# Kernel tuning notes

Hardware: AMD Instinct MI355X
Metric: run time of the kernel (lower is better)

The kernel has to match this reference:

```python
import jax, jax.numpy as jnp
import numpy as np

N, F_IN, H, OUT, E = 1_000_000, 8, 32, 9, 4_000_000


def setup_inputs() -> dict:
    key = jax.random.key(0)
    ks = jax.random.split(key, 32)
    s = 0.05
    inp = {
        "x": jax.random.normal(ks[0], (N, F_IN), jnp.float32),
        "edge_index": jax.random.randint(ks[1], (2, E), 0, N, jnp.int64),
        "edge_weight": jax.random.uniform(ks[2], (E,), jnp.float32),
        "h": jax.random.normal(ks[3], (N, H), jnp.float32),
        "c": jax.random.normal(ks[4], (N, H), jnp.float32),
    }
    i = 5
    # per-gate ChebConv(K=1) weights on x and h, peephole vectors, gate biases
    for g in ["i", "f", "c", "o"]:
        inp[f"Wx{g}"] = jax.random.normal(ks[i], (F_IN, H), jnp.float32) * s; i += 1
        inp[f"bx{g}"] = jnp.zeros((H,), jnp.float32)
        inp[f"Wh{g}"] = jax.random.normal(ks[i], (H, H), jnp.float32) * s; i += 1
        inp[f"bh{g}"] = jnp.zeros((H,), jnp.float32)
        inp[f"b{g}"] = jnp.zeros((H,), jnp.float32)
        if g != "c":  # cell candidate gate has no peephole
            inp[f"wc{g}"] = jax.random.normal(ks[i], (H,), jnp.float32) * s; i += 1
    inp["Wl"] = jax.random.normal(ks[i], (H, OUT), jnp.float32) * s
    inp["bl"] = jnp.zeros((OUT,), jnp.float32)
    return inp


def reference(x, edge_index, edge_weight, h, c,
              Wxi, bxi, Whi, bhi, bi, wci,
              Wxf, bxf, Whf, bhf, bf, wcf,
              Wxc, bxc, Whc, bhc, bc,
              Wxo, bxo, Who, bho, bo, wco,
              Wl, bl):
    # GConvLSTM with ChebConv K=1: graph conv degenerates to x @ W + b
    # (edge_index / edge_weight do not enter the math for K=1).
    i_g = jax.nn.sigmoid(x @ Wxi + bxi + h @ Whi + bhi + wci * c + bi)
    f_g = jax.nn.sigmoid(x @ Wxf + bxf + h @ Whf + bhf + wcf * c + bf)
    t_g = jnp.tanh(x @ Wxc + bxc + h @ Whc + bhc + bc)
    c0 = f_g * c + i_g * t_g
    o_g = jax.nn.sigmoid(x @ Wxo + bxo + h @ Who + bho + wco * c0 + bo)
    h0 = o_g * jnp.tanh(c0)
    y = jax.nn.relu(h0) @ Wl + bl  # [N, 9]
    return (y, h0, c0)
```

## Files before the change

### kernel.cpp

```cpp
#include <hip/hip_runtime.h>
#include <math.h>


#define HD 32
#define FD 8
#define BLK 256

struct Params {
    const float* __restrict__ x;
    const float* __restrict__ h;
    const float* __restrict__ c;
    const float* __restrict__ Wx[4];
    const float* __restrict__ bx[4];
    const float* __restrict__ Wh[4];
    const float* __restrict__ bh[4];
    const float* __restrict__ b[4];
    const float* __restrict__ wci;
    const float* __restrict__ wcf;
    const float* __restrict__ wco;
    const float* __restrict__ Wl;
    const float* __restrict__ bl;
    float* __restrict__ y;
    float* __restrict__ h0;
    float* __restrict__ c0;
    int N;
};

__device__ __forceinline__ float rcp_f(float x) { return __builtin_amdgcn_rcpf(x); }
__device__ __forceinline__ float fsigmoid(float x) { return rcp_f(1.0f + __expf(-x)); }
__device__ __forceinline__ float ftanh(float x) {
    float e = __expf(2.0f * fabsf(x));
    float r = 1.0f - 2.0f * rcp_f(1.0f + e);
    return copysignf(r, x);
}

__global__ __launch_bounds__(BLK) void gconvlstm_kernel(Params p) {
    __shared__ __align__(16) float WXT[4][HD][FD];
    __shared__ __align__(16) float WHT[4][HD][HD];
    __shared__ __align__(16) float WLT[HD][12];
    __shared__ __align__(16) float SCV[HD][8];

    const int tid = threadIdx.x;

    for (int t = tid; t < 4 * HD * FD; t += BLK) {
        int g = t >> 8, r = t & 255, j = r >> 3, k = r & 7;
        WXT[g][j][k] = p.Wx[g][k * HD + j];
    }
    for (int t = tid; t < 4 * HD * HD; t += BLK) {
        int g = t >> 10, r = t & 1023, j = r >> 5, k = r & 31;
        WHT[g][j][k] = p.Wh[g][k * HD + j];
    }
    for (int t = tid; t < HD * 12; t += BLK) {
        int j = t / 12, m = t - j * 12;
        WLT[j][m] = (m < 9) ? p.Wl[j * 9 + m] : 0.0f;
    }
    for (int t = tid; t < HD * 8; t += BLK) {
        int j = t >> 3, s = t & 7;
        float v = 0.0f;
        if (s < 4)      v = p.bx[s][j] + p.bh[s][j] + p.b[s][j];
        else if (s == 4) v = p.wci[j];
        else if (s == 5) v = p.wcf[j];
        else if (s == 6) v = p.wco[j];
        SCV[j][s] = v;
    }
    __syncthreads();

    const int n = blockIdx.x * BLK + tid;
    if (n >= p.N) return;

    float xv[FD], hv[HD], cv[HD], h0a[HD];

    const float4* xp = reinterpret_cast<const float4*>(p.x + (size_t)n * FD);
    reinterpret_cast<float4*>(xv)[0] = xp[0];
    reinterpret_cast<float4*>(xv)[1] = xp[1];
    const float4* hp = reinterpret_cast<const float4*>(p.h + (size_t)n * HD);
#pragma unroll
    for (int q = 0; q < 8; ++q) reinterpret_cast<float4*>(hv)[q] = hp[q];
    const float4* cp = reinterpret_cast<const float4*>(p.c + (size_t)n * HD);
#pragma unroll
    for (int q = 0; q < 8; ++q) reinterpret_cast<float4*>(cv)[q] = cp[q];

    float yacc[9];
#pragma unroll
    for (int m = 0; m < 9; ++m) yacc[m] = p.bl[m];

#pragma unroll
    for (int j = 0; j < HD; ++j) {
        float ai = 0.f, af = 0.f, at = 0.f, ao = 0.f;
#pragma unroll
        for (int k = 0; k < FD; ++k) {
            ai += xv[k] * WXT[0][j][k];
            af += xv[k] * WXT[1][j][k];
            at += xv[k] * WXT[2][j][k];
            ao += xv[k] * WXT[3][j][k];
        }
#pragma unroll
        for (int k = 0; k < HD; ++k) {
            ai += hv[k] * WHT[0][j][k];
            af += hv[k] * WHT[1][j][k];
            at += hv[k] * WHT[2][j][k];
            ao += hv[k] * WHT[3][j][k];
        }
        const float cj = cv[j];
        const float pi = ai + SCV[j][0] + SCV[j][4] * cj;
        const float pf = af + SCV[j][1] + SCV[j][5] * cj;
        const float pt = at + SCV[j][2];
        const float ig = fsigmoid(pi);
        const float fg = fsigmoid(pf);
        const float tg = ftanh(pt);
        const float c0 = fg * cj + ig * tg;
        const float po = ao + SCV[j][3] + SCV[j][6] * c0;
        const float og = fsigmoid(po);
        const float h0 = og * ftanh(c0);
        cv[j] = c0;
        h0a[j] = h0;
        const float rh = fmaxf(h0, 0.0f);
#pragma unroll
        for (int m = 0; m < 9; ++m) yacc[m] += rh * WLT[j][m];
    }

    float* yo = p.y + (size_t)n * 9;
#pragma unroll
    for (int m = 0; m < 9; ++m) yo[m] = yacc[m];
    float4* ho = reinterpret_cast<float4*>(p.h0 + (size_t)n * HD);
#pragma unroll
    for (int q = 0; q < 8; ++q) ho[q] = reinterpret_cast<const float4*>(h0a)[q];
    float4* co = reinterpret_cast<float4*>(p.c0 + (size_t)n * HD);
#pragma unroll
    for (int q = 0; q < 8; ++q) co[q] = reinterpret_cast<const float4*>(cv)[q];
}

extern "C" void kernel_launch(void* const* d_in, const int* in_sizes, int n_in,
                              void* d_out, int out_size, void* d_ws, size_t ws_size,
                              hipStream_t stream) {
    (void)n_in; (void)d_ws; (void)ws_size;
    const int N = in_sizes[0] / FD;

    Params p;
    p.x = (const float*)d_in[0];
    p.h = (const float*)d_in[3];
    p.c = (const float*)d_in[4];

    const int wx_i[4] = {5, 11, 17, 22};
    const int bx_i[4] = {6, 12, 18, 23};
    const int wh_i[4] = {7, 13, 19, 24};
    const int bh_i[4] = {8, 14, 20, 25};
    const int b_i[4]  = {9, 15, 21, 26};
    for (int g = 0; g < 4; ++g) {
        p.Wx[g] = (const float*)d_in[wx_i[g]];
        p.bx[g] = (const float*)d_in[bx_i[g]];
        p.Wh[g] = (const float*)d_in[wh_i[g]];
        p.bh[g] = (const float*)d_in[bh_i[g]];
        p.b[g]  = (const float*)d_in[b_i[g]];
    }
    p.wci = (const float*)d_in[10];
    p.wcf = (const float*)d_in[16];
    p.wco = (const float*)d_in[27];
    p.Wl  = (const float*)d_in[28];
    p.bl  = (const float*)d_in[29];

    float* out = (float*)d_out;
    p.y  = out;
    p.h0 = out + (size_t)9 * N;
    p.c0 = out + (size_t)41 * N;
    p.N  = N;

    const int blocks = (N + BLK - 1) / BLK;
    gconvlstm_kernel<<<blocks, BLK, 0, stream>>>(p);
}
```

Measured before the change: 772.4 us.

## Pre-transpose weights into workspace and read them via uniform scalar loads

A one-block prep kernel transposes and packs all gate weights, fused biases, peepholes and the output layer into a workspace buffer. The main kernel no longer stages weights in shared memory or syncs, and reads them straight from global memory with wave-uniform addresses, which the compiler can turn into scalar loads. The cell state is now streamed one float4 at a time and outputs are written per chunk, which lowers register pressure. tanh also uses a cheaper formula. The cost is an extra kernel launch, plus a heavy dependence on the scalar cache for about 5.7K weight reads per thread.

New measurement: 968.6 us. +25.4%, slower.

```diff
diff --git a/kernel.cpp b/kernel.cpp
--- a/kernel.cpp
+++ b/kernel.cpp
@@ -6,165 +6,166 @@
 #define FD 8
 #define BLK 256
 
-struct Params {
-    const float* __restrict__ x;
-    const float* __restrict__ h;
-    const float* __restrict__ c;
-    const float* __restrict__ Wx[4];
-    const float* __restrict__ bx[4];
-    const float* __restrict__ Wh[4];
-    const float* __restrict__ bh[4];
-    const float* __restrict__ b[4];
-    const float* __restrict__ wci;
-    const float* __restrict__ wcf;
-    const float* __restrict__ wco;
-    const float* __restrict__ Wl;
-    const float* __restrict__ bl;
-    float* __restrict__ y;
-    float* __restrict__ h0;
-    float* __restrict__ c0;
-    int N;
+#define CW_WXT 0
+#define CW_WHT 1024
+#define CW_WL  5120
+#define CW_B   5504
+#define CW_PCI 5632
+#define CW_PCF 5664
+#define CW_PCO 5696
+#define CW_BL  5728
+#define CW_TOT 5740
+
+struct PrepArgs {
+    const float* Wxi; const float* Wxf; const float* Wxc; const float* Wxo;
+    const float* Whi; const float* Whf; const float* Whc; const float* Who;
+    const float* bxi; const float* bxf; const float* bxc; const float* bxo;
+    const float* bhi; const float* bhf; const float* bhc; const float* bho;
+    const float* bi;  const float* bf;  const float* bc;  const float* bo;
+    const float* wci; const float* wcf; const float* wco;
+    const float* Wl;  const float* bl;
 };
 
-__device__ __forceinline__ float rcp_f(float x) { return __builtin_amdgcn_rcpf(x); }
-__device__ __forceinline__ float fsigmoid(float x) { return rcp_f(1.0f + __expf(-x)); }
-__device__ __forceinline__ float ftanh(float x) {
-    float e = __expf(2.0f * fabsf(x));
-    float r = 1.0f - 2.0f * rcp_f(1.0f + e);
-    return copysignf(r, x);
+__global__ __launch_bounds__(256) void prep_kernel(PrepArgs a, float* __restrict__ w) {
+    const int t = threadIdx.x;
+#define DO_WX(G, PTR)                                                     \
+    for (int i = t; i < HD * FD; i += 256) {                              \
+        int j = i >> 3, k = i & 7;                                        \
+        w[CW_WXT + (G) * HD * FD + i] = PTR[k * HD + j];                  \
+    }
+    DO_WX(0, a.Wxi) DO_WX(1, a.Wxf) DO_WX(2, a.Wxc) DO_WX(3, a.Wxo)
+#undef DO_WX
+#define DO_WH(G, PTR)                                                     \
+    for (int i = t; i < HD * HD; i += 256) {                              \
+        int j = i >> 5, k = i & 31;                                       \
+        w[CW_WHT + (G) * HD * HD + i] = PTR[k * HD + j];                  \
+    }
+    DO_WH(0, a.Whi) DO_WH(1, a.Whf) DO_WH(2, a.Whc) DO_WH(3, a.Who)
+#undef DO_WH
+    for (int i = t; i < HD * 12; i += 256) {
+        int j = i / 12, m = i - j * 12;
+        w[CW_WL + i] = (m < 9) ? a.Wl[j * 9 + m] : 0.0f;
+    }
+#define DO_B(G, P1, P2, P3)                                               \
+    for (int i = t; i < HD; i += 256) {                                   \
+        w[CW_B + (G) * HD + i] = P1[i] + P2[i] + P3[i];                   \
+    }
+    DO_B(0, a.bxi, a.bhi, a.bi) DO_B(1, a.bxf, a.bhf, a.bf)
+    DO_B(2, a.bxc, a.bhc, a.bc) DO_B(3, a.bxo, a.bho, a.bo)
+#undef DO_B
+    if (t < HD) {
+        w[CW_PCI + t] = a.wci[t];
+        w[CW_PCF + t] = a.wcf[t];
+        w[CW_PCO + t] = a.wco[t];
+    }
+    if (t < 12) w[CW_BL + t] = (t < 9) ? a.bl[t] : 0.0f;
 }
 
-__global__ __launch_bounds__(BLK) void gconvlstm_kernel(Params p) {
-    __shared__ __align__(16) float WXT[4][HD][FD];
-    __shared__ __align__(16) float WHT[4][HD][HD];
-    __shared__ __align__(16) float WLT[HD][12];
-    __shared__ __align__(16) float SCV[HD][8];
+__device__ __forceinline__ float rcp_f(float v) { return __builtin_amdgcn_rcpf(v); }
+__device__ __forceinline__ float fsigmoid(float v) { return rcp_f(1.0f + __expf(-v)); }
+__device__ __forceinline__ float ftanh(float v) {
+    return __builtin_fmaf(2.0f, rcp_f(1.0f + __expf(-2.0f * v)), -1.0f);
+}
 
-    const int tid = threadIdx.x;
+__global__ __launch_bounds__(BLK) void gconvlstm_main(
+    const float* __restrict__ x, const float* __restrict__ h, const float* __restrict__ c,
+    const float* __restrict__ cw,
+    float* __restrict__ y, float* __restrict__ h0, float* __restrict__ c0, int N)
+{
+    const int n = blockIdx.x * BLK + threadIdx.x;
+    if (n >= N) return;
 
-    for (int t = tid; t < 4 * HD * FD; t += BLK) {
-        int g = t >> 8, r = t & 255, j = r >> 3, k = r & 7;
-        WXT[g][j][k] = p.Wx[g][k * HD + j];
+    float xv[FD];
+    {
+        const float4* xp = reinterpret_cast<const float4*>(x + (size_t)n * FD);
+        reinterpret_cast<float4*>(xv)[0] = xp[0];
+        reinterpret_cast<float4*>(xv)[1] = xp[1];
     }
-    for (int t = tid; t < 4 * HD * HD; t += BLK) {
-        int g = t >> 10, r = t & 1023, j = r >> 5, k = r & 31;
-        WHT[g][j][k] = p.Wh[g][k * HD + j];
+    float hv[HD];
+    {
+        const float4* hp = reinterpret_cast<const float4*>(h + (size_t)n * HD);
+#pragma unroll
+        for (int q = 0; q < 8; ++q) reinterpret_cast<float4*>(hv)[q] = hp[q];
     }
-    for (int t = tid; t < HD * 12; t += BLK) {
-        int j = t / 12, m = t - j * 12;
-        WLT[j][m] = (m < 9) ? p.Wl[j * 9 + m] : 0.0f;
-    }
-    for (int t = tid; t < HD * 8; t += BLK) {
-        int j = t >> 3, s = t & 7;
-        float v = 0.0f;
-        if (s < 4)      v = p.bx[s][j] + p.bh[s][j] + p.b[s][j];
-        else if (s == 4) v = p.wci[j];
-        else if (s == 5) v = p.wcf[j];
-        else if (s == 6) v = p.wco[j];
-        SCV[j][s] = v;
-    }
-    __syncthreads();
-
-    const int n = blockIdx.x * BLK + tid;
-    if (n >= p.N) return;
-
-    float xv[FD], hv[HD], cv[HD], h0a[HD];
-
-    const float4* xp = reinterpret_cast<const float4*>(p.x + (size_t)n * FD);
-    reinterpret_cast<float4*>(xv)[0] = xp[0];
-    reinterpret_cast<float4*>(xv)[1] = xp[1];
-    const float4* hp = reinterpret_cast<const float4*>(p.h + (size_t)n * HD);
-#pragma unroll
-    for (int q = 0; q < 8; ++q) reinterpret_cast<float4*>(hv)[q] = hp[q];
-    const float4* cp = reinterpret_cast<const float4*>(p.c + (size_t)n * HD);
-#pragma unroll
-    for (int q = 0; q < 8; ++q) reinterpret_cast<float4*>(cv)[q] = cp[q];
 
     float yacc[9];
 #pragma unroll
-    for (int m = 0; m < 9; ++m) yacc[m] = p.bl[m];
+    for (int m = 0; m < 9; ++m) yacc[m] = cw[CW_BL + m];
 
+    const float4* cp  = reinterpret_cast<const float4*>(c  + (size_t)n * HD);
+    float4*       hop = reinterpret_cast<float4*>(h0 + (size_t)n * HD);
+    float4*       cop = reinterpret_cast<float4*>(c0 + (size_t)n * HD);
+
+#pragma unroll 1
+    for (int jc = 0; jc < 8; ++jc) {
+        const float4 c4 = cp[jc];
+        float h04[4], c04[4];
 #pragma unroll
-    for (int j = 0; j < HD; ++j) {
-        float ai = 0.f, af = 0.f, at = 0.f, ao = 0.f;
+        for (int jj = 0; jj < 4; ++jj) {
+            const int j = jc * 4 + jj;
+            float ag[4];
 #pragma unroll
-        for (int k = 0; k < FD; ++k) {
-            ai += xv[k] * WXT[0][j][k];
-            af += xv[k] * WXT[1][j][k];
-            at += xv[k] * WXT[2][j][k];
-            ao += xv[k] * WXT[3][j][k];
+            for (int g = 0; g < 4; ++g) {
+                float acc = cw[CW_B + g * HD + j];
+                const float* __restrict__ wx = cw + CW_WXT + (g * HD + j) * FD;
+#pragma unroll
+                for (int k = 0; k < FD; ++k) acc += xv[k] * wx[k];
+                const float* __restrict__ wh = cw + CW_WHT + (g * HD + j) * HD;
+#pragma unroll
+                for (int k = 0; k < HD; ++k) acc += hv[k] * wh[k];
+                ag[g] = acc;
+            }
+            const float cj = (&c4.x)[jj];
+            const float ig = fsigmoid(ag[0] + cw[CW_PCI + j] * cj);
+            const float fg = fsigmoid(ag[1] + cw[CW_PCF + j] * cj);
+            const float tg = ftanh(ag[2]);
+            const float cn = fg * cj + ig * tg;
+            const float og = fsigmoid(ag[3] + cw[CW_PCO + j] * cn);
+            const float hn = og * ftanh(cn);
+            c04[jj] = cn;
+            h04[jj] = hn;
+            const float rh = fmaxf(hn, 0.0f);
+            const float* __restrict__ wl = cw + CW_WL + j * 12;
+#pragma unroll
+            for (int m = 0; m < 9; ++m) yacc[m] += rh * wl[m];
         }
-#pragma unroll
-        for (int k = 0; k < HD; ++k) {
-            ai += hv[k] * WHT[0][j][k];
-            af += hv[k] * WHT[1][j][k];
-            at += hv[k] * WHT[2][j][k];
-            ao += hv[k] * WHT[3][j][k];
-        }
-        const float cj = cv[j];
-        const float pi = ai + SCV[j][0] + SCV[j][4] * cj;
-        const float pf = af + SCV[j][1] + SCV[j][5] * cj;
-        const float pt = at + SCV[j][2];
-        const float ig = fsigmoid(pi);
-        const float fg = fsigmoid(pf);
-        const float tg = ftanh(pt);
-        const float c0 = fg * cj + ig * tg;
-        const float po = ao + SCV[j][3] + SCV[j][6] * c0;
-        const float og = fsigmoid(po);
-        const float h0 = og * ftanh(c0);
-        cv[j] = c0;
-        h0a[j] = h0;
-        const float rh = fmaxf(h0, 0.0f);
-#pragma unroll
-        for (int m = 0; m < 9; ++m) yacc[m] += rh * WLT[j][m];
+        hop[jc] = make_float4(h04[0], h04[1], h04[2], h04[3]);
+        cop[jc] = make_float4(c04[0], c04[1], c04[2], c04[3]);
     }
 
-    float* yo = p.y + (size_t)n * 9;
+    float* yo = y + (size_t)n * 9;
 #pragma unroll
     for (int m = 0; m < 9; ++m) yo[m] = yacc[m];
-    float4* ho = reinterpret_cast<float4*>(p.h0 + (size_t)n * HD);
-#pragma unroll
-    for (int q = 0; q < 8; ++q) ho[q] = reinterpret_cast<const float4*>(h0a)[q];
-    float4* co = reinterpret_cast<float4*>(p.c0 + (size_t)n * HD);
-#pragma unroll
-    for (int q = 0; q < 8; ++q) co[q] = reinterpret_cast<const float4*>(cv)[q];
 }
 
 extern "C" void kernel_launch(void* const* d_in, const int* in_sizes, int n_in,
                               void* d_out, int out_size, void* d_ws, size_t ws_size,
                               hipStream_t stream) {
-    (void)n_in; (void)d_ws; (void)ws_size;
+    (void)n_in; (void)out_size; (void)ws_size;
     const int N = in_sizes[0] / FD;
 
-    Params p;
-    p.x = (const float*)d_in[0];
-    p.h = (const float*)d_in[3];
-    p.c = (const float*)d_in[4];
+    PrepArgs a;
+    a.Wxi = (const float*)d_in[5];  a.bxi = (const float*)d_in[6];
+    a.Whi = (const float*)d_in[7];  a.bhi = (const float*)d_in[8];
+    a.bi  = (const float*)d_in[9];  a.wci = (const float*)d_in[10];
+    a.Wxf = (const float*)d_in[11]; a.bxf = (const float*)d_in[12];
+    a.Whf = (const float*)d_in[13]; a.bhf = (const float*)d_in[14];
+    a.bf  = (const float*)d_in[15]; a.wcf = (const float*)d_in[16];
+    a.Wxc = (const float*)d_in[17]; a.bxc = (const float*)d_in[18];
+    a.Whc = (const float*)d_in[19]; a.bhc = (const float*)d_in[20];
+    a.bc  = (const float*)d_in[21];
+    a.Wxo = (const float*)d_in[22]; a.bxo = (const float*)d_in[23];
+    a.Who = (const float*)d_in[24]; a.bho = (const float*)d_in[25];
+    a.bo  = (const float*)d_in[26]; a.wco = (const float*)d_in[27];
+    a.Wl  = (const float*)d_in[28]; a.bl  = (const float*)d_in[29];
 
-    const int wx_i[4] = {5, 11, 17, 22};
-    const int bx_i[4] = {6, 12, 18, 23};
-    const int wh_i[4] = {7, 13, 19, 24};
-    const int bh_i[4] = {8, 14, 20, 25};
-    const int b_i[4]  = {9, 15, 21, 26};
-    for (int g = 0; g < 4; ++g) {
-        p.Wx[g] = (const float*)d_in[wx_i[g]];
-        p.bx[g] = (const float*)d_in[bx_i[g]];
-        p.Wh[g] = (const float*)d_in[wh_i[g]];
-        p.bh[g] = (const float*)d_in[bh_i[g]];
-        p.b[g]  = (const float*)d_in[b_i[g]];
-    }
-    p.wci = (const float*)d_in[10];
-    p.wcf = (const float*)d_in[16];
-    p.wco = (const float*)d_in[27];
-    p.Wl  = (const float*)d_in[28];
-    p.bl  = (const float*)d_in[29];
+    float* ws = (float*)d_ws;
+    prep_kernel<<<1, 256, 0, stream>>>(a, ws);
 
     float* out = (float*)d_out;
-    p.y  = out;
-    p.h0 = out + (size_t)9 * N;
-    p.c0 = out + (size_t)41 * N;
-    p.N  = N;
-
     const int blocks = (N + BLK - 1) / BLK;
-    gconvlstm_kernel<<<blocks, BLK, 0, stream>>>(p);
+    gconvlstm_main<<<blocks, BLK, 0, stream>>>(
+        (const float*)d_in[0], (const float*)d_in[3], (const float*)d_in[4],
+        ws,
+        out, out + (size_t)9 * N, out + (size_t)41 * N, N);
 }
```
